# Performance work log

Measured on AMD Instinct MI355X. Metric: run time of the kernel, lower is better.

## Reference

```python
import jax, jax.numpy as jnp
import numpy as np

QLEN, MLEN, BSZ, D_MODEL, N_HEAD, D_HEAD = 1024, 1024, 4, 1024, 16, 64
KLEN = QLEN + MLEN
LN_EPS = 1e-5


def _linear(x, W, b):
    return x @ W + b


def _layer_norm(x, g, b):
    mu = jnp.mean(x, axis=-1, keepdims=True)
    var = jnp.var(x, axis=-1, keepdims=True)
    return (x - mu) * jax.lax.rsqrt(var + LN_EPS) * g + b


def _rel_shift(x):
    # x: [b, n, q, k] -> Transformer-XL rel-shift via zero-pad + reshape trick
    b, n, q, k = x.shape
    x = jnp.pad(x, ((0, 0), (0, 0), (0, 0), (1, 0)))
    x = x.reshape(b, n, k + 1, q)[:, :, 1:, :].reshape(b, n, q, k)
    return x


def setup_inputs() -> dict:
    key = jax.random.key(0)
    ks = jax.random.split(key, 16)
    s = 0.02
    inp = {
        "w": jax.random.normal(ks[0], (QLEN, BSZ, D_MODEL), jnp.float32),
        "r": jax.random.normal(ks[1], (KLEN, D_MODEL), jnp.float32),
        "r_w_bias": jax.random.normal(ks[2], (N_HEAD, D_HEAD), jnp.float32) * s,
        "r_r_bias": jax.random.normal(ks[3], (N_HEAD, D_HEAD), jnp.float32) * s,
        "mems": jax.random.normal(ks[4], (MLEN, BSZ, D_MODEL), jnp.float32),
        "Wq": jax.random.normal(ks[5], (D_MODEL, N_HEAD * D_HEAD), jnp.float32) * s,
        "bq": jnp.zeros((N_HEAD * D_HEAD,), jnp.float32),
        "Wk": jax.random.normal(ks[6], (D_MODEL, N_HEAD * D_HEAD), jnp.float32) * s,
        "bk": jnp.zeros((N_HEAD * D_HEAD,), jnp.float32),
        "Wv": jax.random.normal(ks[7], (D_MODEL, N_HEAD * D_HEAD), jnp.float32) * s,
        "bv": jnp.zeros((N_HEAD * D_HEAD,), jnp.float32),
        "Wr": jax.random.normal(ks[8], (D_MODEL, N_HEAD * D_HEAD), jnp.float32) * s,
        "br": jnp.zeros((N_HEAD * D_HEAD,), jnp.float32),
        "Wo": jax.random.normal(ks[9], (N_HEAD * D_HEAD, D_MODEL), jnp.float32) * s,
        "bo": jnp.zeros((D_MODEL,), jnp.float32),
        "ln_g": jnp.ones((D_MODEL,), jnp.float32),
        "ln_b": jnp.zeros((D_MODEL,), jnp.float32),
    }
    # causal mask with memory: key j visible to query i iff j <= i + MLEN
    inp["attn_mask"] = jnp.arange(KLEN)[None, :] > (jnp.arange(QLEN)[:, None] + MLEN)
    return inp


def reference(w, r, r_w_bias, r_r_bias, mems, Wq, bq, Wk, bk, Wv, bv, Wr, br,
              Wo, bo, ln_g, ln_b, attn_mask):
    qlen, bsz = w.shape[0], w.shape[1]
    scale = 1.0 / (D_HEAD ** 0.5)

    cat = jnp.concatenate([mems, w], axis=0)               # [klen, b, d]
    klen = cat.shape[0]

    q = _linear(cat, Wq, bq)[-qlen:]                       # [q, b, n*d]
    k = _linear(cat, Wk, bk)                               # [k, b, n*d]
    v = _linear(cat, Wv, bv)
    rk = _linear(r, Wr, br)                                # [rlen, n*d]

    q = q.reshape(qlen, bsz, N_HEAD, D_HEAD)
    k = k.reshape(klen, bsz, N_HEAD, D_HEAD)
    v = v.reshape(klen, bsz, N_HEAD, D_HEAD)
    rk = rk.reshape(r.shape[0], N_HEAD, D_HEAD)

    AC = jnp.einsum('ibnd,jbnd->bnij', q + r_w_bias, k)
    BD = jnp.einsum('ibnd,jnd->bnij', q + r_r_bias, rk)
    BD = _rel_shift(BD)

    attn_score = scale * (AC + BD)                          # [b, n, q, k]
    attn_score = jnp.where(attn_mask[None, None, :, :], -jnp.inf, attn_score)
    attn_prob = jax.nn.softmax(attn_score, axis=3)

    attn_vec = jnp.einsum('bnij,jbnd->ibnd', attn_prob, v)
    attn_vec = attn_vec.reshape(qlen, bsz, N_HEAD * D_HEAD)
    attn_out = _linear(attn_vec, Wo, bo)

    return _layer_norm(w + attn_out, ln_g, ln_b)            # post-lnorm path
```

## Files before the change

### kernel.cpp

```cpp
#include <hip/hip_runtime.h>
#include <stdint.h>


typedef unsigned short u16;
typedef unsigned int u32;
typedef __attribute__((ext_vector_type(8))) short s16x8;
typedef __attribute__((ext_vector_type(4))) float f32x4;

typedef const __attribute__((address_space(1))) void gvoid;
typedef __attribute__((address_space(3))) void lvoid;

__device__ __forceinline__ void async16(const u16* g, u16* l) {
  __builtin_amdgcn_global_load_lds((gvoid*)g, (lvoid*)l, 16, 0, 0);
}

__device__ __forceinline__ float b2f(u16 h) {
  union { u32 u; float f; } v; v.u = ((u32)h) << 16; return v.f;
}
__device__ __forceinline__ u16 f2b(float f) {
  union { float f; u32 u; } v; v.f = f; u32 u = v.u;
  return (u16)((u + 0x7FFFu + ((u >> 16) & 1u)) >> 16);
}
__device__ __forceinline__ bool is_bf16(const u16* lng) { return lng[0] == 0x3F80u; }

__device__ __forceinline__ void ld8(const void* p, size_t idx, bool bf, u16* dst) {
  if (bf) {
    *(uint4*)dst = *(const uint4*)((const u16*)p + idx);
  } else {
    const float* f = (const float*)p + idx;
    float4 a = *(const float4*)f;
    float4 c = *(const float4*)(f + 4);
    dst[0] = f2b(a.x); dst[1] = f2b(a.y); dst[2] = f2b(a.z); dst[3] = f2b(a.w);
    dst[4] = f2b(c.x); dst[5] = f2b(c.y); dst[6] = f2b(c.z); dst[7] = f2b(c.w);
  }
}
__device__ __forceinline__ float ldS(const void* p, int idx, bool bf) {
  return bf ? b2f(((const u16*)p)[idx]) : ((const float*)p)[idx];
}

__device__ __forceinline__ void gemm256_bt_body(
    u16* As, u16* Bs,
    const void* Alo, const void* Ahi, int splitRow,
    const u16* BT, const void* bias,
    const void* eb0, const void* eb1,
    u16* C0, u16* C1, bool bfin, bool abf,
    int bm, int bnc)
{
  const int t = threadIdx.x;
  const int lane = t & 63, w = t >> 6;
  const int wm = w >> 2, wn = w & 3;
  const int ml = lane & 15, q = lane >> 4;

  f32x4 zero4 = {0.f, 0.f, 0.f, 0.f};
  f32x4 acc[8][4];
#pragma unroll
  for (int i = 0; i < 8; ++i)
#pragma unroll
    for (int j = 0; j < 4; ++j) acc[i][j] = zero4;

  const int srow = t >> 3;
  const int scol = ((t & 7) ^ ((t >> 3) & 7)) << 3;
  const void* aptr[4]; size_t aidx[4]; const u16* bsrc[4];
#pragma unroll
  for (int p = 0; p < 4; ++p) {
    int gr = bm + p * 64 + srow;
    if (gr < splitRow) { aptr[p] = Alo; aidx[p] = (size_t)gr * 1024 + scol; }
    else { aptr[p] = Ahi; aidx[p] = (size_t)(gr - splitRow) * 1024 + scol; }
    bsrc[p] = BT + (size_t)(bnc + p * 64 + srow) * 1024 + scol;
  }
  u16* lA[4]; u16* lB[4];
#pragma unroll
  for (int p = 0; p < 4; ++p) { lA[p] = As + p * 4096 + t * 8; lB[p] = Bs + p * 4096 + t * 8; }

  for (int kk = 0; kk < 1024; kk += 64) {
    __syncthreads();
    if (abf) {
#pragma unroll
      for (int p = 0; p < 4; ++p) {
        async16((const u16*)aptr[p] + aidx[p] + kk, lA[p]);
        async16(bsrc[p] + kk, lB[p]);
      }
    } else {
      u16 ta[4][8]; uint4 tb[4];
#pragma unroll
      for (int p = 0; p < 4; ++p) {
        ld8(aptr[p], aidx[p] + kk, false, ta[p]);
        tb[p] = *(const uint4*)(bsrc[p] + kk);
      }
#pragma unroll
      for (int p = 0; p < 4; ++p) {
        *(uint4*)lA[p] = *(uint4*)ta[p];
        *(uint4*)lB[p] = tb[p];
      }
    }
    __syncthreads();
#pragma unroll
    for (int ki = 0; ki < 2; ++ki) {
      const int rc = (((ki << 2) + q) ^ (ml & 7)) << 3;
      s16x8 af[8], bf[4];
#pragma unroll
      for (int mi = 0; mi < 8; ++mi)
        af[mi] = *(const s16x8*)&As[(wm * 128 + mi * 16 + ml) * 64 + rc];
#pragma unroll
      for (int ni = 0; ni < 4; ++ni)
        bf[ni] = *(const s16x8*)&Bs[(wn * 64 + ni * 16 + ml) * 64 + rc];
#pragma unroll
      for (int mi = 0; mi < 8; ++mi)
#pragma unroll
        for (int ni = 0; ni < 4; ++ni)
          acc[mi][ni] = __builtin_amdgcn_mfma_f32_16x16x32_bf16(af[mi], bf[ni],
                                                                acc[mi][ni], 0, 0, 0);
    }
  }

#pragma unroll
  for (int ni = 0; ni < 4; ++ni) {
    int gcol = bnc + wn * 64 + ni * 16 + ml;
    float bi = ldS(bias, gcol, bfin);
    float e0 = eb0 ? ldS(eb0, gcol, bfin) : 0.f;
    float e1 = eb1 ? ldS(eb1, gcol, bfin) : 0.f;
#pragma unroll
    for (int mi = 0; mi < 8; ++mi)
#pragma unroll
      for (int rr = 0; rr < 4; ++rr) {
        int grow = bm + wm * 128 + mi * 16 + 4 * q + rr;
        size_t off = (size_t)grow * 1024 + gcol;
        float v0 = acc[mi][ni][rr] + bi;
        if (C1) { C0[off] = f2b(v0 + e0); C1[off] = f2b(v0 + e1); }
        else    { C0[off] = f2b(v0); }
      }
  }
}

__device__ __forceinline__ void gemm256_vt_body(
    u16* As, u16* Bs,
    const void* Mlo, const void* Whi,
    const u16* WvT, const void* bv,
    u16* vT, bool bfin,
    int j0, int nc0, int b)
{
  const int t = threadIdx.x;
  const int lane = t & 63, w = t >> 6;
  const int wm = w >> 2, wn = w & 3;
  const int ml = lane & 15, q = lane >> 4;

  f32x4 zero4 = {0.f, 0.f, 0.f, 0.f};
  f32x4 acc[8][4];
#pragma unroll
  for (int i = 0; i < 8; ++i)
#pragma unroll
    for (int j = 0; j < 4; ++j) acc[i][j] = zero4;

  const int srow = t >> 3;
  const int scol = ((t & 7) ^ ((t >> 3) & 7)) << 3;
  const u16* asrc[4]; const void* bptr[4]; size_t bidx[4];
#pragma unroll
  for (int p = 0; p < 4; ++p) {
    asrc[p] = WvT + (size_t)(nc0 + p * 64 + srow) * 1024 + scol;
    int j = j0 + p * 64 + srow;
    if (j < 1024) { bptr[p] = Mlo; bidx[p] = ((size_t)j * 4 + b) * 1024 + scol; }
    else { bptr[p] = Whi; bidx[p] = ((size_t)(j - 1024) * 4 + b) * 1024 + scol; }
  }
  u16* lA[4]; u16* lB[4];
#pragma unroll
  for (int p = 0; p < 4; ++p) { lA[p] = As + p * 4096 + t * 8; lB[p] = Bs + p * 4096 + t * 8; }

  for (int kk = 0; kk < 1024; kk += 64) {
    __syncthreads();
    if (bfin) {
#pragma unroll
      for (int p = 0; p < 4; ++p) {
        async16(asrc[p] + kk, lA[p]);
        async16((const u16*)bptr[p] + bidx[p] + kk, lB[p]);
      }
    } else {
      u16 tb[4][8];
#pragma unroll
      for (int p = 0; p < 4; ++p) ld8(bptr[p], bidx[p] + kk, false, tb[p]);
#pragma unroll
      for (int p = 0; p < 4; ++p) {
        async16(asrc[p] + kk, lA[p]);
        *(uint4*)lB[p] = *(uint4*)tb[p];
      }
    }
    __syncthreads();
#pragma unroll
    for (int ki = 0; ki < 2; ++ki) {
      const int rc = (((ki << 2) + q) ^ (ml & 7)) << 3;
      s16x8 af[8], bf[4];
#pragma unroll
      for (int mi = 0; mi < 8; ++mi)
        af[mi] = *(const s16x8*)&As[(wm * 128 + mi * 16 + ml) * 64 + rc];
#pragma unroll
      for (int ni = 0; ni < 4; ++ni)
        bf[ni] = *(const s16x8*)&Bs[(wn * 64 + ni * 16 + ml) * 64 + rc];
#pragma unroll
      for (int mi = 0; mi < 8; ++mi)
#pragma unroll
        for (int ni = 0; ni < 4; ++ni)
          acc[mi][ni] = __builtin_amdgcn_mfma_f32_16x16x32_bf16(af[mi], bf[ni],
                                                                acc[mi][ni], 0, 0, 0);
    }
  }

#pragma unroll
  for (int mi = 0; mi < 8; ++mi)
#pragma unroll
    for (int rr = 0; rr < 4; ++rr) {
      int nc = nc0 + wm * 128 + mi * 16 + 4 * q + rr;
      float bi = ldS(bv, nc, bfin);
      size_t rbase = ((size_t)b * 1024 + nc) * 2048 + j0 + wn * 64 + ml * 4;
      u32 w0 = (u32)f2b(acc[mi][0][rr] + bi) | ((u32)f2b(acc[mi][1][rr] + bi) << 16);
      u32 w1 = (u32)f2b(acc[mi][2][rr] + bi) | ((u32)f2b(acc[mi][3][rr] + bi) << 16);
      uint2 pk; pk.x = w0; pk.y = w1;
      *(uint2*)(vT + rbase) = pk;
    }
}

__global__ __launch_bounds__(512, 2) void proj_uber256(
    const void* __restrict__ mems, const void* __restrict__ w,
    const void* __restrict__ r,
    const u16* __restrict__ WkT, const void* __restrict__ bk,
    const u16* __restrict__ WvT, const void* __restrict__ bv,
    const u16* __restrict__ WqT, const void* __restrict__ bq,
    const void* __restrict__ rwb, const void* __restrict__ rrb,
    const u16* __restrict__ WrT, const void* __restrict__ br,
    u16* __restrict__ kb, u16* __restrict__ vT,
    u16* __restrict__ qw, u16* __restrict__ qr, u16* __restrict__ rkb,
    const u16* __restrict__ lng)
{
  __shared__ u16 As[256 * 64];
  __shared__ u16 Bs[256 * 64];
  const bool bfin = is_bf16(lng);
  int id = blockIdx.x;
  id = (id & 7) * 44 + (id >> 3);

  if (id < 128) {
    int bx = id & 3, by = id >> 2;
    gemm256_bt_body(As, Bs, mems, w, 4096, WkT, bk, nullptr, nullptr,
                    kb, nullptr, bfin, bfin, by * 256, bx * 256);
  } else if (id < 256) {
    int local = id - 128;
    int jx = local & 7, ny = (local >> 3) & 3, b = local >> 5;
    gemm256_vt_body(As, Bs, mems, w, WvT, bv, vT, bfin, jx * 256, ny * 256, b);
  } else if (id < 320) {
    int local = id - 256;
    int bx = local & 3, by = local >> 2;
    gemm256_bt_body(As, Bs, w, w, 1 << 30, WqT, bq, rwb, rrb,
                    qw, qr, bfin, bfin, by * 256, bx * 256);
  } else {
    int local = id - 320;
    int bx = local & 3, by = local >> 2;
    gemm256_bt_body(As, Bs, r, r, 1 << 30, WrT, br, nullptr, nullptr,
                    rkb, nullptr, bfin, bfin, by * 256, bx * 256);
  }
}

__device__ __forceinline__ void gemm_bt_body(
    u16* As, u16* Bs,
    const void* Alo, const void* Ahi, int splitRow,
    const u16* BT, const void* bias,
    const void* eb0, const void* eb1,
    u16* C0, u16* C1, bool bfin, bool abf,
    int bm, int bnc)
{
  const int t = threadIdx.x;
  const int lane = t & 63, w = t >> 6;
  const int wr = w >> 1, wc = w & 1;
  const int ml = lane & 15, q = lane >> 4;

  f32x4 zero4 = {0.f, 0.f, 0.f, 0.f};
  f32x4 acc[4][4];
#pragma unroll
  for (int i = 0; i < 4; ++i)
#pragma unroll
    for (int j = 0; j < 4; ++j) acc[i][j] = zero4;

  const int srow = t >> 2;
  const int sch  = t & 3;
  const void* aptr[2]; size_t aidx[2]; const u16* bsrc[2];
#pragma unroll
  for (int p = 0; p < 2; ++p) {
    int gr = bm + srow + p * 64;
    if (gr < splitRow) { aptr[p] = Alo; aidx[p] = (size_t)gr * 1024 + sch * 8; }
    else { aptr[p] = Ahi; aidx[p] = (size_t)(gr - splitRow) * 1024 + sch * 8; }
    bsrc[p] = BT + (size_t)(bnc + srow + p * 64) * 1024 + sch * 8;
  }
  u16* lA[2] = { As + t * 8, As + 2048 + t * 8 };
  u16* lB[2] = { Bs + t * 8, Bs + 2048 + t * 8 };

  for (int kk = 0; kk < 1024; kk += 32) {
    if (abf) {
      __syncthreads();
      async16((const u16*)aptr[0] + aidx[0] + kk, lA[0]);
      async16((const u16*)aptr[1] + aidx[1] + kk, lA[1]);
      async16(bsrc[0] + kk, lB[0]);
      async16(bsrc[1] + kk, lB[1]);
      __syncthreads();
    } else {
      u16 ta0[8], ta1[8];
      ld8(aptr[0], aidx[0] + kk, false, ta0);
      ld8(aptr[1], aidx[1] + kk, false, ta1);
      uint4 vb0 = *(const uint4*)(bsrc[0] + kk);
      uint4 vb1 = *(const uint4*)(bsrc[1] + kk);
      __syncthreads();
      *(uint4*)lA[0] = *(uint4*)ta0;
      *(uint4*)lA[1] = *(uint4*)ta1;
      *(uint4*)lB[0] = vb0;
      *(uint4*)lB[1] = vb1;
      __syncthreads();
    }
    s16x8 af[4], bf[4];
#pragma unroll
    for (int mi = 0; mi < 4; ++mi)
      af[mi] = *(const s16x8*)&As[(wr * 64 + mi * 16 + ml) * 32 + q * 8];
#pragma unroll
    for (int ni = 0; ni < 4; ++ni)
      bf[ni] = *(const s16x8*)&Bs[(wc * 64 + ni * 16 + ml) * 32 + q * 8];
#pragma unroll
    for (int mi = 0; mi < 4; ++mi)
#pragma unroll
      for (int ni = 0; ni < 4; ++ni)
        acc[mi][ni] = __builtin_amdgcn_mfma_f32_16x16x32_bf16(af[mi], bf[ni],
                                                              acc[mi][ni], 0, 0, 0);
  }

#pragma unroll
  for (int ni = 0; ni < 4; ++ni) {
    int gcol = bnc + wc * 64 + ni * 16 + ml;
    float bi = ldS(bias, gcol, bfin);
    float e0 = eb0 ? ldS(eb0, gcol, bfin) : 0.f;
    float e1 = eb1 ? ldS(eb1, gcol, bfin) : 0.f;
#pragma unroll
    for (int mi = 0; mi < 4; ++mi)
#pragma unroll
      for (int rr = 0; rr < 4; ++rr) {
        int grow = bm + wr * 64 + mi * 16 + 4 * q + rr;
        size_t off = (size_t)grow * 1024 + gcol;
        float v0 = acc[mi][ni][rr] + bi;
        if (C1) { C0[off] = f2b(v0 + e0); C1[off] = f2b(v0 + e1); }
        else    { C0[off] = f2b(v0); }
      }
  }
}

__global__ __launch_bounds__(256) void gemm_bt(
    const void* __restrict__ Alo, const void* __restrict__ Ahi, int splitRow,
    const u16* __restrict__ BT, const void* __restrict__ bias,
    const void* __restrict__ eb0, const void* __restrict__ eb1,
    u16* __restrict__ C0, u16* __restrict__ C1,
    const u16* __restrict__ lng, int aIsInput)
{
  __shared__ u16 As[128 * 32];
  __shared__ u16 Bs[128 * 32];
  const bool bfin = is_bf16(lng);
  const bool abf = aIsInput ? bfin : true;
  int lin = blockIdx.y * gridDim.x + blockIdx.x;
  int nwg = gridDim.x * gridDim.y;
  int cpx = nwg >> 3;
  int id  = (lin & 7) * cpx + (lin >> 3);
  int bx = id % gridDim.x, by = id / gridDim.x;
  gemm_bt_body(As, Bs, Alo, Ahi, splitRow, BT, bias, eb0, eb1, C0, C1,
               bfin, abf, by * 128, bx * 128);
}

__global__ __launch_bounds__(256) void transpose_w5(
    const void* __restrict__ W0, const void* __restrict__ W1,
    const void* __restrict__ W2, const void* __restrict__ W3,
    const void* __restrict__ W4,
    u16* __restrict__ T0, u16* __restrict__ T1, u16* __restrict__ T2,
    u16* __restrict__ T3, u16* __restrict__ T4, const u16* __restrict__ lng)
{
  __shared__ u16 tile[64 * 72];
  const bool bf = is_bf16(lng);
  const void* W; u16* T;
  switch (blockIdx.z) {
    case 0: W = W0; T = T0; break;
    case 1: W = W1; T = T1; break;
    case 2: W = W2; T = T2; break;
    case 3: W = W3; T = T3; break;
    default: W = W4; T = T4; break;
  }
  const int t = threadIdx.x;
  const int k0 = blockIdx.y * 64, n0 = blockIdx.x * 64;
#pragma unroll
  for (int p = 0; p < 2; ++p) {
    int s = p * 256 + t, row = s >> 3, ch = s & 7;
    u16 tmp[8];
    ld8(W, (size_t)(k0 + row) * 1024 + n0 + ch * 8, bf, tmp);
    *(uint4*)&tile[row * 72 + ch * 8] = *(uint4*)tmp;
  }
  __syncthreads();
#pragma unroll
  for (int p = 0; p < 2; ++p) {
    int s = p * 256 + t, nrow = s >> 3, ch = s & 7;
    union { u16 u[8]; uint4 v; } pk;
#pragma unroll
    for (int jj = 0; jj < 8; ++jj) pk.u[jj] = tile[(ch * 8 + jj) * 72 + nrow];
    *(uint4*)(T + (size_t)(n0 + nrow) * 1024 + k0 + ch * 8) = pk.v;
  }
}

__global__ __launch_bounds__(512, 4) void flash_attn(
    const u16* __restrict__ qw, const u16* __restrict__ qr,
    const u16* __restrict__ kb, const u16* __restrict__ vt,
    const u16* __restrict__ rkb, u16* __restrict__ av)
{
  constexpr int LP = 72;
  __shared__ u16 Ks[64 * LP];
  __shared__ u16 Vs[64 * LP];
  __shared__ u16 Rs[192 * LP];
  __shared__ u16 Ps[8][16 * LP];

  const int t = threadIdx.x;
  const int lane = t & 63, w = t >> 6;
  const int ml = lane & 15, q = lane >> 4;
  const int hbid = blockIdx.y * 8 + blockIdx.x;
  const int lbid = (hbid & 7) * 64 + (hbid >> 3);
  const int L = lbid & 63;
  const int i0idx = (L < 32) ? (L & 7) : 7 - (L & 7);
  const int i0 = i0idx * 128;
  const int bn = lbid >> 3, b = bn >> 4, nh = bn & 15;

  s16x8 aqw[2], aqr[2];
  {
    size_t qo = ((size_t)(i0 + 16 * w + ml) * 4 + b) * 1024 + nh * 64 + q * 8;
    aqw[0] = *(const s16x8*)(qw + qo);
    aqw[1] = *(const s16x8*)(qw + qo + 32);
    aqr[0] = *(const s16x8*)(qr + qo);
    aqr[1] = *(const s16x8*)(qr + qo + 32);
  }

  f32x4 zero4 = {0.f, 0.f, 0.f, 0.f};
  f32x4 o[4];
#pragma unroll
  for (int dt = 0; dt < 4; ++dt) o[dt] = zero4;
  float lsum[4] = {0.f, 0.f, 0.f, 0.f};

  const int ntiles = min(i0 / 64 + 18, 32);
  const int c_lo = 16 * (7 - w);
  const int srow = t >> 3, sch = t & 7;

  uint4 pK, pV, pR;
  auto issue_kv = [&](int jt) {
    const int j0n = jt * 64;
    pK = *(const uint4*)(kb + ((size_t)(j0n + srow) * 4 + b) * 1024 + nh * 64 + sch * 8);
    pV = *(const uint4*)(vt + ((size_t)bn * 64 + srow) * 2048 + j0n + sch * 8);
  };
  auto rload = [&](int g) {
    g = g < 0 ? 0 : (g > 2047 ? 2047 : g);
    return *(const uint4*)(rkb + (size_t)g * 1024 + nh * 64 + sch * 8);
  };

  {
    issue_kv(0);
    uint4 r0 = rload(896 - i0 + srow);
    uint4 r1 = rload(896 - i0 + srow + 64);
    uint4 r2 = rload(896 - i0 + srow + 128);
    *(uint4*)&Ks[srow * LP + sch * 8] = pK;
    *(uint4*)&Vs[srow * LP + sch * 8] = pV;
    *(uint4*)&Rs[(srow      ) * LP + sch * 8] = r0;
    *(uint4*)&Rs[(srow +  64) * LP + sch * 8] = r1;
    *(uint4*)&Rs[(srow + 128) * LP + sch * 8] = r2;
  }
  __syncthreads();

  int slab = 0;
  int rbase = c_lo;
  for (int jt = 0; jt < ntiles; ++jt) {
    const int j0 = jt * 64;
    if (jt > 0) {
      __syncthreads();
      *(uint4*)&Ks[srow * LP + sch * 8] = pK;
      *(uint4*)&Vs[srow * LP + sch * 8] = pV;
      *(uint4*)&Rs[(slab * 64 + srow) * LP + sch * 8] = pR;
      slab = slab == 2 ? 0 : slab + 1;
      rbase += 64; if (rbase >= 192) rbase -= 192;
      __syncthreads();
    }
    if (jt + 1 < ntiles) {
      issue_kv(jt + 1);
      pR = rload(64 * jt + 1088 - i0 + srow);
    }

    __builtin_amdgcn_s_setprio(1);
    f32x4 sac[4];
#pragma unroll
    for (int tt = 0; tt < 4; ++tt) sac[tt] = zero4;
#pragma unroll
    for (int ki = 0; ki < 2; ++ki)
#pragma unroll
      for (int tt = 0; tt < 4; ++tt) {
        s16x8 bfr = *(const s16x8*)&Ks[(tt * 16 + ml) * LP + ki * 32 + q * 8];
        sac[tt] = __builtin_amdgcn_mfma_f32_16x16x32_bf16(aqw[ki], bfr, sac[tt], 0, 0, 0);
      }

    f32x4 g[5];
#pragma unroll
    for (int ct = 0; ct < 5; ++ct) g[ct] = zero4;
#pragma unroll
    for (int ct = 0; ct < 5; ++ct) {
      int pb = rbase + ct * 16; if (pb >= 192) pb -= 192;
      const u16* rp = &Rs[(pb + ml) * LP + q * 8];
      s16x8 b0 = *(const s16x8*)(rp);
      s16x8 b1 = *(const s16x8*)(rp + 32);
      g[ct] = __builtin_amdgcn_mfma_f32_16x16x32_bf16(aqr[0], b0, g[ct], 0, 0, 0);
      g[ct] = __builtin_amdgcn_mfma_f32_16x16x32_bf16(aqr[1], b1, g[ct], 0, 0, 0);
    }
    __builtin_amdgcn_s_setprio(0);

    const bool mtile = (j0 + 63) > (i0 + 1024);

#pragma unroll
    for (int rr = 0; rr < 4; ++rr) {
      const int r = 4 * q + rr;
      const int irow = i0 + 16 * w + r;
      const int L2 = ((ml - r + 15) & 15) | (q << 4);
      const bool hs = ml < 15 - r;
      float bl0 = hs ? g[1][rr] : g[0][rr];
      float bl1 = hs ? g[2][rr] : g[1][rr];
      float bl2 = hs ? g[3][rr] : g[2][rr];
      float bl3 = hs ? g[4][rr] : g[3][rr];
      float band0 = __shfl(bl0, L2, 64);
      float band1 = __shfl(bl1, L2, 64);
      float band2 = __shfl(bl2, L2, 64);
      float band3 = __shfl(bl3, L2, 64);
      float s0 = 0.125f * (sac[0][rr] + band0);
      float s1 = 0.125f * (sac[1][rr] + band1);
      float s2 = 0.125f * (sac[2][rr] + band2);
      float s3 = 0.125f * (sac[3][rr] + band3);
      if (mtile) {
        int lim = irow + 1024 - j0 - ml;
        if (0 > lim)  s0 = -3.0e38f;
        if (16 > lim) s1 = -3.0e38f;
        if (32 > lim) s2 = -3.0e38f;
        if (48 > lim) s3 = -3.0e38f;
      }
      float p0 = __expf(s0), p1 = __expf(s1), p2 = __expf(s2), p3 = __expf(s3);
      lsum[rr] += (p0 + p1) + (p2 + p3);
      u32 w0 = (u32)f2b(p0) | ((u32)f2b(p1) << 16);
      u32 w1 = (u32)f2b(p2) | ((u32)f2b(p3) << 16);
      uint2 pk; pk.x = w0; pk.y = w1;
      *(uint2*)&Ps[w][r * LP + ml * 4] = pk;
    }

    __builtin_amdgcn_s_setprio(1);
#pragma unroll
    for (int ki = 0; ki < 2; ++ki) {
      s16x8 a = *(const s16x8*)&Ps[w][ml * LP + ki * 32 + q * 8];
#pragma unroll
      for (int dt = 0; dt < 4; ++dt) {
        s16x8 bfr = *(const s16x8*)&Vs[(dt * 16 + ml) * LP + ki * 32 + q * 8];
        o[dt] = __builtin_amdgcn_mfma_f32_16x16x32_bf16(a, bfr, o[dt], 0, 0, 0);
      }
    }
    __builtin_amdgcn_s_setprio(0);
  }

#pragma unroll
  for (int rr = 0; rr < 4; ++rr) {
    float l = lsum[rr];
#pragma unroll
    for (int off = 1; off < 16; off <<= 1) l += __shfl_xor(l, off);
    float inv = 1.f / l;
    int i = i0 + 16 * w + 4 * q + rr;
#pragma unroll
    for (int dt = 0; dt < 4; ++dt)
      av[((size_t)i * 4 + b) * 1024 + nh * 64 + dt * 16 + ml] = f2b(o[dt][rr] * inv);
  }
}

__global__ __launch_bounds__(256) void ln_kernel(
    const void* __restrict__ wi, const u16* __restrict__ ao,
    const void* __restrict__ gg, const void* __restrict__ bb,
    void* __restrict__ out)
{
  __shared__ float red[8];
  const bool bf = is_bf16((const u16*)gg);
  const int t = threadIdx.x;
  const int row = blockIdx.x;
  const int base = row * 1024 + t * 4;
  float x0, x1, x2, x3;
  if (bf) {
    ushort4 xw = *(const ushort4*)((const u16*)wi + base);
    x0 = b2f(xw.x); x1 = b2f(xw.y); x2 = b2f(xw.z); x3 = b2f(xw.w);
  } else {
    float4 xw = *(const float4*)((const float*)wi + base);
    x0 = xw.x; x1 = xw.y; x2 = xw.z; x3 = xw.w;
  }
  ushort4 xa = *(const ushort4*)(ao + base);
  x0 += b2f(xa.x); x1 += b2f(xa.y); x2 += b2f(xa.z); x3 += b2f(xa.w);
  float s = x0 + x1 + x2 + x3;
  float s2 = x0 * x0 + x1 * x1 + x2 * x2 + x3 * x3;
#pragma unroll
  for (int off = 1; off < 64; off <<= 1) {
    s += __shfl_xor(s, off);
    s2 += __shfl_xor(s2, off);
  }
  if ((t & 63) == 0) { red[t >> 6] = s; red[4 + (t >> 6)] = s2; }
  __syncthreads();
  float S = red[0] + red[1] + red[2] + red[3];
  float S2 = red[4] + red[5] + red[6] + red[7];
  float mu = S * (1.f / 1024.f);
  float var = S2 * (1.f / 1024.f) - mu * mu;
  float inv = rsqrtf(var + 1e-5f);
  float g0 = ldS(gg, t * 4 + 0, bf), g1 = ldS(gg, t * 4 + 1, bf);
  float g2 = ldS(gg, t * 4 + 2, bf), g3 = ldS(gg, t * 4 + 3, bf);
  float b0 = ldS(bb, t * 4 + 0, bf), b1 = ldS(bb, t * 4 + 1, bf);
  float b2v = ldS(bb, t * 4 + 2, bf), b3 = ldS(bb, t * 4 + 3, bf);
  float y0 = (x0 - mu) * inv * g0 + b0;
  float y1 = (x1 - mu) * inv * g1 + b1;
  float y2 = (x2 - mu) * inv * g2 + b2v;
  float y3 = (x3 - mu) * inv * g3 + b3;
  if (bf) {
    ushort4 r;
    r.x = f2b(y0); r.y = f2b(y1); r.z = f2b(y2); r.w = f2b(y3);
    *(ushort4*)((u16*)out + base) = r;
  } else {
    float4 r; r.x = y0; r.y = y1; r.z = y2; r.w = y3;
    *(float4*)((float*)out + base) = r;
  }
}

__global__ __launch_bounds__(256) void copy_w(
    const void* __restrict__ wi, const u16* __restrict__ lng,
    void* __restrict__ out)
{
  const bool bf = is_bf16(lng);
  int i = blockIdx.x * 256 + threadIdx.x;
  if (bf) ((u16*)out)[i] = ((const u16*)wi)[i];
  else    ((float*)out)[i] = ((const float*)wi)[i];
}

extern "C" void kernel_launch(void* const* d_in, const int* in_sizes, int n_in,
                              void* d_out, int out_size, void* d_ws, size_t ws_size,
                              hipStream_t stream) {
  (void)in_sizes; (void)n_in; (void)out_size;
  const void* w    = d_in[0];
  const void* r    = d_in[1];
  const void* rwb  = d_in[2];
  const void* rrb  = d_in[3];
  const void* mems = d_in[4];
  const void* Wq   = d_in[5];
  const void* bq   = d_in[6];
  const void* Wk   = d_in[7];
  const void* bk   = d_in[8];
  const void* Wv   = d_in[9];
  const void* bv   = d_in[10];
  const void* Wr   = d_in[11];
  const void* br   = d_in[12];
  const void* Wo   = d_in[13];
  const void* bo   = d_in[14];
  const u16*  lng  = (const u16*)d_in[15];
  const void* lnb  = d_in[16];

  dim3 blk(256);
  const size_t M = (size_t)1 << 20;
  const size_t NEED = 31 * M * 2;
  if (ws_size < NEED) {
    copy_w<<<dim3(16384), blk, 0, stream>>>(w, lng, d_out);
    return;
  }

  u16* ws  = (u16*)d_ws;
  u16* WqT = ws + 0 * M;
  u16* WkT = ws + 1 * M;
  u16* WvT = ws + 2 * M;
  u16* WrT = ws + 3 * M;
  u16* WoT = ws + 4 * M;
  u16* kb  = ws + 5 * M;
  u16* vT  = ws + 13 * M;
  u16* qw  = ws + 21 * M;
  u16* qr  = ws + 25 * M;
  u16* rkb = ws + 29 * M;
  u16* av  = ws + 0 * M;
  u16* ao  = qw;

  transpose_w5<<<dim3(16, 16, 5), blk, 0, stream>>>(Wq, Wk, Wv, Wr, Wo,
                                                    WqT, WkT, WvT, WrT, WoT, lng);
  proj_uber256<<<dim3(352), dim3(512), 0, stream>>>(mems, w, r,
                                                    WkT, bk, WvT, bv, WqT, bq,
                                                    rwb, rrb, WrT, br,
                                                    kb, vT, qw, qr, rkb, lng);
  flash_attn<<<dim3(8, 64), dim3(512), 0, stream>>>(qw, qr, kb, vT, rkb, av);
  gemm_bt<<<dim3(8, 32), blk, 0, stream>>>(av, av, 1 << 30, WoT, bo,
                                           nullptr, nullptr, ao, nullptr, lng, 0);
  ln_kernel<<<dim3(4096), blk, 0, stream>>>(w, ao, lng, lnb, d_out);
}
```

Before: 357.4 us.

## Double-buffer LDS tiles with async prefetch in projection GEMMs

The bf16-input path of the fused projection kernel now uses two LDS buffers. It prefetches the next two K-tiles with global_load_lds, waits with explicit vmcnt counts, and raises wave priority around the MFMA block, so global loads overlap compute instead of being serialized with barriers. The fp32-input path issues its global loads before the barrier so they overlap the previous tile's compute. Shared memory per block doubles to 128KB, which likely prevents two blocks per CU and lowers occupancy. With fp32 inputs the new pipelined path may not run at all.

Result: slower. 398.2 us (+11.4%).

```diff
diff --git a/kernel.cpp b/kernel.cpp
--- a/kernel.cpp
+++ b/kernel.cpp
@@ -38,7 +38,7 @@
   return bf ? b2f(((const u16*)p)[idx]) : ((const float*)p)[idx];
 }
 
-__device__ __forceinline__ void gemm256_bt_body(
+__device__ __forceinline__ void gemm256p_bt_body(
     u16* As, u16* Bs,
     const void* Alo, const void* Ahi, int splitRow,
     const u16* BT, const void* bias,
@@ -68,48 +68,87 @@
     else { aptr[p] = Ahi; aidx[p] = (size_t)(gr - splitRow) * 1024 + scol; }
     bsrc[p] = BT + (size_t)(bnc + p * 64 + srow) * 1024 + scol;
   }
-  u16* lA[4]; u16* lB[4];
-#pragma unroll
-  for (int p = 0; p < 4; ++p) { lA[p] = As + p * 4096 + t * 8; lB[p] = Bs + p * 4096 + t * 8; }
-
-  for (int kk = 0; kk < 1024; kk += 64) {
-    __syncthreads();
-    if (abf) {
+
+  if (abf) {
+    auto STAGE = [&](int buf, int kk) {
+      u16* a = As + buf * 16384 + t * 8;
+      u16* b = Bs + buf * 16384 + t * 8;
 #pragma unroll
       for (int p = 0; p < 4; ++p) {
-        async16((const u16*)aptr[p] + aidx[p] + kk, lA[p]);
-        async16(bsrc[p] + kk, lB[p]);
-      }
-    } else {
+        async16((const u16*)aptr[p] + aidx[p] + kk, a + p * 4096);
+        async16(bsrc[p] + kk, b + p * 4096);
+      }
+    };
+    STAGE(0, 0);
+    STAGE(1, 64);
+    asm volatile("s_waitcnt vmcnt(8)" ::: "memory");
+    __builtin_amdgcn_s_barrier();
+    int cur = 0;
+    for (int kt = 0; kt < 16; ++kt) {
+      const u16* Ab = As + cur * 16384;
+      const u16* Bb = Bs + cur * 16384;
+      __builtin_amdgcn_s_setprio(1);
+#pragma unroll
+      for (int ki = 0; ki < 2; ++ki) {
+        const int rc = (((ki << 2) + q) ^ (ml & 7)) << 3;
+        s16x8 af[8], bf[4];
+#pragma unroll
+        for (int mi = 0; mi < 8; ++mi)
+          af[mi] = *(const s16x8*)&Ab[(wm * 128 + mi * 16 + ml) * 64 + rc];
+#pragma unroll
+        for (int ni = 0; ni < 4; ++ni)
+          bf[ni] = *(const s16x8*)&Bb[(wn * 64 + ni * 16 + ml) * 64 + rc];
+#pragma unroll
+        for (int mi = 0; mi < 8; ++mi)
+#pragma unroll
+          for (int ni = 0; ni < 4; ++ni)
+            acc[mi][ni] = __builtin_amdgcn_mfma_f32_16x16x32_bf16(af[mi], bf[ni],
+                                                                  acc[mi][ni], 0, 0, 0);
+      }
+      __builtin_amdgcn_s_setprio(0);
+      __builtin_amdgcn_s_barrier();
+      if (kt + 2 < 16) {
+        STAGE(cur, (kt + 2) * 64);
+        asm volatile("s_waitcnt vmcnt(8)" ::: "memory");
+      } else {
+        asm volatile("s_waitcnt vmcnt(0)" ::: "memory");
+      }
+      __builtin_amdgcn_s_barrier();
+      cur ^= 1;
+    }
+  } else {
+    for (int kk = 0; kk < 1024; kk += 64) {
       u16 ta[4][8]; uint4 tb[4];
 #pragma unroll
       for (int p = 0; p < 4; ++p) {
         ld8(aptr[p], aidx[p] + kk, false, ta[p]);
         tb[p] = *(const uint4*)(bsrc[p] + kk);
       }
+      __syncthreads();
 #pragma unroll
       for (int p = 0; p < 4; ++p) {
-        *(uint4*)lA[p] = *(uint4*)ta[p];
-        *(uint4*)lB[p] = tb[p];
-      }
-    }
-    __syncthreads();
-#pragma unroll
-    for (int ki = 0; ki < 2; ++ki) {
-      const int rc = (((ki << 2) + q) ^ (ml & 7)) << 3;
-      s16x8 af[8], bf[4];
-#pragma unroll
-      for (int mi = 0; mi < 8; ++mi)
-        af[mi] = *(const s16x8*)&As[(wm * 128 + mi * 16 + ml) * 64 + rc];
-#pragma unroll
-      for (int ni = 0; ni < 4; ++ni)
-        bf[ni] = *(const s16x8*)&Bs[(wn * 64 + ni * 16 + ml) * 64 + rc];
-#pragma unroll
-      for (int mi = 0; mi < 8; ++mi)
+        *(uint4*)(As + p * 4096 + t * 8) = *(uint4*)ta[p];
+        *(uint4*)(Bs + p * 4096 + t * 8) = tb[p];
+      }
+      __syncthreads();
+#pragma unroll
+      for (int ki = 0; ki < 2; ++ki) {
+        const int rc = (((ki << 2) + q) ^ (ml & 7)) << 3;
+        s16x8 af[8], bf[4];
+#pragma unroll
+        for (int mi = 0; mi < 8; ++mi)
+          af[mi] = *(const s16x8*)&As[(wm * 128 + mi * 16 + ml) * 64 + rc];
 #pragma unroll
         for (int ni = 0; ni < 4; ++ni)
-          acc[mi][ni] = __builtin_amdgcn_mfma_f32_16x16x32_bf16(af[mi], bf[ni],
-                                                                acc[mi][ni], 0, 0, 0);
+          bf[ni] = *(const s16x8*)&Bs[(wn * 64 + ni * 16 + ml) * 64 + rc];
+#pragma unroll
+        for (int mi = 0; mi < 8; ++mi)
+#pragma unroll
+          for (int ni = 0; ni < 4; ++ni)
+            acc[mi][ni] = __builtin_amdgcn_mfma_f32_16x16x32_bf16(af[mi], bf[ni],
+                                                                  acc[mi][ni], 0, 0, 0);
+      }
+      __syncthreads();
     }
   }
 
@@ -132,7 +171,7 @@
   }
 }
 
-__device__ __forceinline__ void gemm256_vt_body(
+__device__ __forceinline__ void gemm256p_vt_body(
     u16* As, u16* Bs,
     const void* Mlo, const void* Whi,
     const u16* WvT, const void* bv,
@@ -161,45 +200,84 @@
     if (j < 1024) { bptr[p] = Mlo; bidx[p] = ((size_t)j * 4 + b) * 1024 + scol; }
     else { bptr[p] = Whi; bidx[p] = ((size_t)(j - 1024) * 4 + b) * 1024 + scol; }
   }
-  u16* lA[4]; u16* lB[4];
-#pragma unroll
-  for (int p = 0; p < 4; ++p) { lA[p] = As + p * 4096 + t * 8; lB[p] = Bs + p * 4096 + t * 8; }
-
-  for (int kk = 0; kk < 1024; kk += 64) {
-    __syncthreads();
-    if (bfin) {
+
+  if (bfin) {
+    auto STAGE = [&](int buf, int kk) {
+      u16* a = As + buf * 16384 + t * 8;
+      u16* b2 = Bs + buf * 16384 + t * 8;
 #pragma unroll
       for (int p = 0; p < 4; ++p) {
-        async16(asrc[p] + kk, lA[p]);
-        async16((const u16*)bptr[p] + bidx[p] + kk, lB[p]);
-      }
-    } else {
+        async16(asrc[p] + kk, a + p * 4096);
+        async16((const u16*)bptr[p] + bidx[p] + kk, b2 + p * 4096);
+      }
+    };
+    STAGE(0, 0);
+    STAGE(1, 64);
+    asm volatile("s_waitcnt vmcnt(8)" ::: "memory");
+    __builtin_amdgcn_s_barrier();
+    int cur = 0;
+    for (int kt = 0; kt < 16; ++kt) {
+      const u16* Ab = As + cur * 16384;
+      const u16* Bb = Bs + cur * 16384;
+      __builtin_amdgcn_s_setprio(1);
+#pragma unroll
+      for (int ki = 0; ki < 2; ++ki) {
+        const int rc = (((ki << 2) + q) ^ (ml & 7)) << 3;
+        s16x8 af[8], bf[4];
+#pragma unroll
+        for (int mi = 0; mi < 8; ++mi)
+          af[mi] = *(const s16x8*)&Ab[(wm * 128 + mi * 16 + ml) * 64 + rc];
+#pragma unroll
+        for (int ni = 0; ni < 4; ++ni)
+          bf[ni] = *(const s16x8*)&Bb[(wn * 64 + ni * 16 + ml) * 64 + rc];
+#pragma unroll
+        for (int mi = 0; mi < 8; ++mi)
+#pragma unroll
+          for (int ni = 0; ni < 4; ++ni)
+            acc[mi][ni] = __builtin_amdgcn_mfma_f32_16x16x32_bf16(af[mi], bf[ni],
+                                                                  acc[mi][ni], 0, 0, 0);
+      }
+      __builtin_amdgcn_s_setprio(0);
+      __builtin_amdgcn_s_barrier();
+      if (kt + 2 < 16) {
+        STAGE(cur, (kt + 2) * 64);
+        asm volatile("s_waitcnt vmcnt(8)" ::: "memory");
+      } else {
+        asm volatile("s_waitcnt vmcnt(0)" ::: "memory");
+      }
+      __builtin_amdgcn_s_barrier();
+      cur ^= 1;
+    }
+  } else {
+    for (int kk = 0; kk < 1024; kk += 64) {
       u16 tb[4][8];
 #pragma unroll
       for (int p = 0; p < 4; ++p) ld8(bptr[p], bidx[p] + kk, false, tb[p]);
+      __syncthreads();
 #pragma unroll
       for (int p = 0; p < 4; ++p) {
-        async16(asrc[p] + kk, lA[p]);
-        *(uint4*)lB[p] = *(uint4*)tb[p];
-      }
-    }
-    __syncthreads();
-#pragma unroll
-    for (int ki = 0; ki < 2; ++ki) {
-      const int rc = (((ki << 2) + q) ^ (ml & 7)) << 3;
-      s16x8 af[8], bf[4];
-#pragma unroll
-      for (int mi = 0; mi < 8; ++mi)
-        af[mi] = *(const s16x8*)&As[(wm * 128 + mi * 16 + ml) * 64 + rc];
-#pragma unroll
-      for (int ni = 0; ni < 4; ++ni)
-        bf[ni] = *(const s16x8*)&Bs[(wn * 64 + ni * 16 + ml) * 64 + rc];
-#pragma unroll
-      for (int mi = 0; mi < 8; ++mi)
+        async16(asrc[p] + kk, As + p * 4096 + t * 8);
+        *(uint4*)(Bs + p * 4096 + t * 8) = *(uint4*)tb[p];
+      }
+      __syncthreads();
+#pragma unroll
+      for (int ki = 0; ki < 2; ++ki) {
+        const int rc = (((ki << 2) + q) ^ (ml & 7)) << 3;
+        s16x8 af[8], bf[4];
+#pragma unroll
+        for (int mi = 0; mi < 8; ++mi)
+          af[mi] = *(const s16x8*)&As[(wm * 128 + mi * 16 + ml) * 64 + rc];
 #pragma unroll
         for (int ni = 0; ni < 4; ++ni)
-          acc[mi][ni] = __builtin_amdgcn_mfma_f32_16x16x32_bf16(af[mi], bf[ni],
-                                                                acc[mi][ni], 0, 0, 0);
+          bf[ni] = *(const s16x8*)&Bs[(wn * 64 + ni * 16 + ml) * 64 + rc];
+#pragma unroll
+        for (int mi = 0; mi < 8; ++mi)
+#pragma unroll
+          for (int ni = 0; ni < 4; ++ni)
+            acc[mi][ni] = __builtin_amdgcn_mfma_f32_16x16x32_bf16(af[mi], bf[ni],
+                                                                  acc[mi][ni], 0, 0, 0);
+      }
+      __syncthreads();
     }
   }
 
@@ -217,7 +295,7 @@
     }
 }
 
-__global__ __launch_bounds__(512, 2) void proj_uber256(
+__global__ __launch_bounds__(512, 2) void proj_uber256p(
     const void* __restrict__ mems, const void* __restrict__ w,
     const void* __restrict__ r,
     const u16* __restrict__ WkT, const void* __restrict__ bk,
@@ -229,30 +307,30 @@
     u16* __restrict__ qw, u16* __restrict__ qr, u16* __restrict__ rkb,
     const u16* __restrict__ lng)
 {
-  __shared__ u16 As[256 * 64];
-  __shared__ u16 Bs[256 * 64];
+  __shared__ u16 As[2 * 16384];
+  __shared__ u16 Bs[2 * 16384];
   const bool bfin = is_bf16(lng);
   int id = blockIdx.x;
   id = (id & 7) * 44 + (id >> 3);
 
   if (id < 128) {
     int bx = id & 3, by = id >> 2;
-    gemm256_bt_body(As, Bs, mems, w, 4096, WkT, bk, nullptr, nullptr,
-                    kb, nullptr, bfin, bfin, by * 256, bx * 256);
+    gemm256p_bt_body(As, Bs, mems, w, 4096, WkT, bk, nullptr, nullptr,
+                     kb, nullptr, bfin, bfin, by * 256, bx * 256);
   } else if (id < 256) {
     int local = id - 128;
     int jx = local & 7, ny = (local >> 3) & 3, b = local >> 5;
-    gemm256_vt_body(As, Bs, mems, w, WvT, bv, vT, bfin, jx * 256, ny * 256, b);
+    gemm256p_vt_body(As, Bs, mems, w, WvT, bv, vT, bfin, jx * 256, ny * 256, b);
   } else if (id < 320) {
     int local = id - 256;
     int bx = local & 3, by = local >> 2;
-    gemm256_bt_body(As, Bs, w, w, 1 << 30, WqT, bq, rwb, rrb,
-                    qw, qr, bfin, bfin, by * 256, bx * 256);
+    gemm256p_bt_body(As, Bs, w, w, 1 << 30, WqT, bq, rwb, rrb,
+                     qw, qr, bfin, bfin, by * 256, bx * 256);
   } else {
     int local = id - 320;
     int bx = local & 3, by = local >> 2;
-    gemm256_bt_body(As, Bs, r, r, 1 << 30, WrT, br, nullptr, nullptr,
-                    rkb, nullptr, bfin, bfin, by * 256, bx * 256);
+    gemm256p_bt_body(As, Bs, r, r, 1 << 30, WrT, br, nullptr, nullptr,
+                     rkb, nullptr, bfin, bfin, by * 256, bx * 256);
   }
 }
 
@@ -678,10 +756,10 @@
 
   transpose_w5<<<dim3(16, 16, 5), blk, 0, stream>>>(Wq, Wk, Wv, Wr, Wo,
                                                     WqT, WkT, WvT, WrT, WoT, lng);
-  proj_uber256<<<dim3(352), dim3(512), 0, stream>>>(mems, w, r,
-                                                    WkT, bk, WvT, bv, WqT, bq,
-                                                    rwb, rrb, WrT, br,
-                                                    kb, vT, qw, qr, rkb, lng);
+  proj_uber256p<<<dim3(352), dim3(512), 0, stream>>>(mems, w, r,
+                                                     WkT, bk, WvT, bv, WqT, bq,
+                                                     rwb, rrb, WrT, br,
+                                                     kb, vT, qw, qr, rkb, lng);
   flash_attn<<<dim3(8, 64), dim3(512), 0, stream>>>(qw, qr, kb, vT, rkb, av);
   gemm_bt<<<dim3(8, 32), blk, 0, stream>>>(av, av, 1 << 30, WoT, bo,
                                            nullptr, nullptr, ao, nullptr, lng, 0);
```
